# Performance work log

Hardware: AMD Instinct MI355X
Metric: run time of the kernel (lower is better)

The kernel has to match this reference:

```python
import jax, jax.numpy as jnp
import numpy as np

B, N, D = 2, 2048, 1024
H, DH = 16, 64
THETA = 10000.0


def setup_inputs() -> dict:
    key = jax.random.key(0)
    k1, k2, k3, k4 = jax.random.split(key, 4)
    hidden_states = jax.random.normal(k1, (B, N, D), dtype=jnp.float32)
    # to_qkv: Linear(D, 3*H*DH, bias=False); stored as [in, out]
    w_qkv = jax.random.normal(k2, (D, 3 * H * DH), dtype=jnp.float32) * (1.0 / np.sqrt(D))
    # to_out: Linear(H*DH, D) with bias (torch default)
    w_out = jax.random.normal(k3, (H * DH, D), dtype=jnp.float32) * (1.0 / np.sqrt(H * DH))
    b_out = jax.random.normal(k4, (D,), dtype=jnp.float32) * 0.01
    return {"hidden_states": hidden_states, "w_qkv": w_qkv, "w_out": w_out, "b_out": b_out}


def _rope_cos_sin(n, dh, dtype):
    # lucidrains RotaryEmbedding: interleaved pairs, theta=10000
    inv_freq = 1.0 / (THETA ** (jnp.arange(0, dh, 2, dtype=jnp.float32) / dh))  # [dh/2]
    t = jnp.arange(n, dtype=jnp.float32)
    freqs = t[:, None] * inv_freq[None, :]                 # [n, dh/2]
    freqs = jnp.repeat(freqs, 2, axis=-1)                  # [n, dh] interleaved
    return jnp.cos(freqs).astype(dtype), jnp.sin(freqs).astype(dtype)


def _rotate_half(x):
    # interleaved: (..., d) -> pairs (x1, x2) -> (-x2, x1)
    x = x.reshape(*x.shape[:-1], -1, 2)
    x1, x2 = x[..., 0], x[..., 1]
    return jnp.stack([-x2, x1], axis=-1).reshape(*x.shape[:-2], -1)


def reference(hidden_states, w_qkv, w_out, b_out):
    b, n, d = hidden_states.shape
    qkv = hidden_states @ w_qkv                            # [b, n, 3*H*DH]
    q, k, v = jnp.split(qkv, 3, axis=-1)
    # b n (h d) -> b h n d
    to_heads = lambda t: t.reshape(b, n, H, DH).transpose(0, 2, 1, 3)
    q, k, v = to_heads(q), to_heads(k), to_heads(v)
    cos, sin = _rope_cos_sin(n, DH, q.dtype)               # [n, DH]
    q = q * cos + _rotate_half(q) * sin
    k = k * cos + _rotate_half(k) * sin
    scale = 1.0 / np.sqrt(DH)
    scores = jnp.einsum('bhqd,bhkd->bhqk', q, k) * scale   # [b, h, n, n]
    attn = jax.nn.softmax(scores, axis=-1)
    out = jnp.einsum('bhqk,bhkd->bhqd', attn, v)           # [b, h, n, DH]
    out = out.transpose(0, 2, 1, 3).reshape(b, n, H * DH)  # b h n d -> b n (h d)
    return out @ w_out + b_out
```

## Files before the change

### kernel.cpp

```cpp
#include <hip/hip_runtime.h>
#include <hip/hip_bf16.h>

typedef __bf16 bf16;
typedef unsigned int u32;
typedef __attribute__((ext_vector_type(4))) float f32x4;
typedef __attribute__((ext_vector_type(16))) float f32x16;
typedef __attribute__((ext_vector_type(8))) bf16 bf16x8;
typedef __attribute__((ext_vector_type(4))) bf16 bf16x4;
typedef __attribute__((ext_vector_type(2))) bf16 bf16x2;
typedef __attribute__((ext_vector_type(4))) u32 u32x4;
typedef __attribute__((ext_vector_type(2))) u32 u32x2;

#define GPTR(p) ((const __attribute__((address_space(1))) u32*)(p))
#define SPTR(p) ((__attribute__((address_space(3))) u32*)(p))

#if __has_builtin(__builtin_amdgcn_permlane32_swap)
#define HAVE_PLSWAP 1
#else
#define HAVE_PLSWAP 0
#endif
#if __has_builtin(__builtin_amdgcn_fdot2_f32_bf16)
#define HAVE_DOT2 1
#else
#define HAVE_DOT2 0
#endif

constexpr int BATCH = 2, SEQ = 2048, DMODEL = 1024, NH = 16, HD = 64, QKV3 = 3072;
constexpr int MTOK = BATCH * SEQ;

constexpr size_t OXB = 0;
constexpr size_t OWQ = OXB + (size_t)MTOK * DMODEL * 2;
constexpr size_t OWO = OWQ + (size_t)QKV3 * DMODEL * 2;
constexpr size_t OCS = OWO + (size_t)DMODEL * DMODEL * 2;
constexpr size_t OCQ = OCS + (size_t)SEQ * 32 * 8;
constexpr size_t OQR = OCQ + (size_t)MTOK * QKV3 * 2;
constexpr size_t OKR = OQR + (size_t)BATCH * NH * SEQ * HD * 2;
constexpr size_t OVT = OKR + (size_t)BATCH * NH * SEQ * HD * 2;
constexpr size_t OAO = OXB;

static __device__ __forceinline__ bf16 tobf(float x) { return (bf16)x; }
static __device__ __forceinline__ float tof(bf16 x) { return (float)x; }

static __device__ __forceinline__ f32x4 mfma16(bf16x8 a, bf16x8 b, f32x4 c) {
  return __builtin_amdgcn_mfma_f32_16x16x32_bf16(a, b, c, 0, 0, 0);
}
static __device__ __forceinline__ f32x16 mfma32(bf16x8 a, bf16x8 b, f32x16 c) {
  return __builtin_amdgcn_mfma_f32_32x32x16_bf16(a, b, c, 0, 0, 0);
}

__global__ void k_prep(const float* __restrict__ hs, const float* __restrict__ wqkv,
                       float* __restrict__ cs, bf16* __restrict__ Xb,
                       bf16* __restrict__ Wqkt) {
  __shared__ float tile[32][33];
  int blk = blockIdx.x, tid = threadIdx.x;
  if (blk < 256) {
    int idx = blk * 256 + tid;
    int n = idx >> 5, i = idx & 31;
    float freq = powf(10000.0f, -(float)(2 * i) / 64.0f);
    float ang = (float)n * freq;
    float s, c;
    sincosf(ang, &s, &c);
    cs[idx * 2] = c;
    cs[idx * 2 + 1] = s;
  } else if (blk < 256 + 4096) {
    int i = (blk - 256) * 256 + tid;
    float4 v = ((const float4*)hs)[i];
    bf16x4 o = {tobf(v.x), tobf(v.y), tobf(v.z), tobf(v.w)};
    ((bf16x4*)Xb)[i] = o;
  } else {
    int t = blk - 4352;
    int n0 = (t % 96) * 32, k0 = (t / 96) * 32;
    int tx = tid & 31, ty = tid >> 5;
#pragma unroll
    for (int r = ty; r < 32; r += 8) tile[r][tx] = wqkv[(size_t)(k0 + r) * QKV3 + n0 + tx];
    __syncthreads();
#pragma unroll
    for (int r = ty; r < 32; r += 8) Wqkt[(size_t)(n0 + r) * DMODEL + k0 + tx] = tobf(tile[tx][r]);
  }
}


__global__ __launch_bounds__(256) void k_gemm2(const bf16* __restrict__ A, const bf16* __restrict__ Bt,
                                               float* __restrict__ C, const float* __restrict__ bias,
                                               int M, int Nn, int K) {
  __shared__ __attribute__((aligned(16))) char smem[36864];
  const int nTn = Nn >> 7;
  int nwg = gridDim.x;
  int bid = blockIdx.x;
  int wgs = (bid & 7) * (nwg >> 3) + (bid >> 3);
  const int m0 = (wgs / nTn) << 6;
  const int n0 = (wgs % nTn) << 7;
  const int tid = threadIdx.x;
  const int lane = tid & 63, w = tid >> 6;
  const int wr = w >> 1, wc = w & 1;
  const int l15 = lane & 15, lhi = lane >> 4;
  f32x4 acc[2][4] = {};

  const int fA = tid * 16;
  const int rA = fA >> 6;
  const int keA = (((fA & 63) >> 4) ^ ((rA >> 1) & 3)) << 3;
  const int fB0 = tid * 16, fB1 = fB0 + 4096;
  const int rB0 = fB0 >> 6, rB1 = fB1 >> 6;
  const int keB0 = (((fB0 & 63) >> 4) ^ ((rB0 >> 1) & 3)) << 3;
  const int keB1 = (((fB1 & 63) >> 4) ^ ((rB1 >> 1) & 3)) << 3;
  const int rsw = ((l15 >> 1) & 3) << 3;

#define GSTAGE(bb_, k0_)                                                                       \
  do {                                                                                         \
    __builtin_amdgcn_global_load_lds(GPTR(A + (size_t)(m0 + rA) * K + (k0_) + keA),            \
                                     SPTR(smem + (bb_)*12288 + fA), 16, 0, 0);                 \
    __builtin_amdgcn_global_load_lds(GPTR(Bt + (size_t)(n0 + rB0) * K + (k0_) + keB0),         \
                                     SPTR(smem + (bb_)*12288 + 4096 + fB0), 16, 0, 0);         \
    __builtin_amdgcn_global_load_lds(GPTR(Bt + (size_t)(n0 + rB1) * K + (k0_) + keB1),         \
                                     SPTR(smem + (bb_)*12288 + 4096 + fB1), 16, 0, 0);         \
  } while (0)

  GSTAGE(0, 0);
  GSTAGE(1, 32);
  const int nIt = K >> 5;
  int bi = 0, b2 = 2;
  for (int it = 0; it < nIt; ++it) {
    if (it < nIt - 1) {
      asm volatile("s_waitcnt vmcnt(3)" ::: "memory");
    } else {
      asm volatile("s_waitcnt vmcnt(0)" ::: "memory");
    }
    __builtin_amdgcn_s_barrier();
    if (it + 2 < nIt) GSTAGE(b2, (it + 2) << 5);
    const bf16* As = (const bf16*)(smem + bi * 12288);
    const bf16* Bs = (const bf16*)(smem + bi * 12288 + 4096);
    bf16x8 af[2], bfv[4];
#pragma unroll
    for (int i = 0; i < 2; ++i)
      af[i] = *(const bf16x8*)(As + (wr * 32 + i * 16 + l15) * 32 + ((lhi << 3) ^ rsw));
#pragma unroll
    for (int j = 0; j < 4; ++j)
      bfv[j] = *(const bf16x8*)(Bs + (wc * 64 + j * 16 + l15) * 32 + ((lhi << 3) ^ rsw));
    __builtin_amdgcn_s_setprio(1);
#pragma unroll
    for (int i = 0; i < 2; ++i)
#pragma unroll
      for (int j = 0; j < 4; ++j) acc[i][j] = mfma16(af[i], bfv[j], acc[i][j]);
    __builtin_amdgcn_s_setprio(0);
    bi = (bi == 2) ? 0 : bi + 1;
    b2 = (b2 == 2) ? 0 : b2 + 1;
  }
#undef GSTAGE

  float bj[4];
#pragma unroll
  for (int j = 0; j < 4; ++j) bj[j] = bias[n0 + wc * 64 + j * 16 + l15];
#pragma unroll
  for (int i = 0; i < 2; ++i)
#pragma unroll
    for (int j = 0; j < 4; ++j) {
      int row = m0 + wr * 32 + i * 16 + lhi * 4;
      int col = n0 + wc * 64 + j * 16 + l15;
#pragma unroll
      for (int r = 0; r < 4; ++r) C[(size_t)(row + r) * Nn + col] = acc[i][j][r] + bj[j];
    }
}


__global__ __launch_bounds__(256) void k_gemm1f(const bf16* __restrict__ A, const bf16* __restrict__ Bt,
                                                const float* __restrict__ cs,
                                                const float* __restrict__ wout, bf16* __restrict__ Woutt,
                                                bf16* __restrict__ Qr, bf16* __restrict__ Kr,
                                                bf16* __restrict__ Vt) {
  constexpr int K = DMODEL, Nn = QKV3;
  constexpr int NG = (MTOK / 128) * (QKV3 / 128);
  __shared__ __attribute__((aligned(16))) char smem[49152];
  int bid = blockIdx.x;
  const int tid = threadIdx.x;

  if (bid >= NG) {
    float* tile = (float*)smem;
    int t = bid - NG;
    int n0 = (t & 31) * 32, k0 = (t >> 5) * 32;
    int tx = tid & 31, ty = tid >> 5;
#pragma unroll
    for (int r = ty; r < 32; r += 8) tile[r * 33 + tx] = wout[(size_t)(k0 + r) * DMODEL + n0 + tx];
    __syncthreads();
#pragma unroll
    for (int r = ty; r < 32; r += 8) Woutt[(size_t)(n0 + r) * DMODEL + k0 + tx] = tobf(tile[tx * 33 + r]);
    return;
  }

  const int nTn = Nn >> 7;
  int wgs = (bid & 7) * (NG >> 3) + (bid >> 3);
  const int m0 = (wgs / nTn) << 7;
  const int n0 = (wgs % nTn) << 7;
  const int lane = tid & 63, w = tid >> 6;
  const int wr = w >> 1, wc = w & 1;
  const int l15 = lane & 15, lhi = lane >> 4;
  f32x4 acc[4][4] = {};

  const int flat0 = w * 1024 + lane * 16;
  const int flat1 = flat0 + 4096;
  const int row0 = flat0 >> 6, row1 = flat1 >> 6;
  const int ke0 = (((flat0 & 63) >> 4) ^ ((row0 >> 1) & 3)) << 3;
  const int ke1 = (((flat1 & 63) >> 4) ^ ((row1 >> 1) & 3)) << 3;
  const int rsw = ((l15 >> 1) & 3) << 3;

#define GSTAGE(bb_, k0_)                                                                       \
  do {                                                                                         \
    __builtin_amdgcn_global_load_lds(GPTR(A + (size_t)(m0 + row0) * K + (k0_) + ke0),          \
                                     SPTR(smem + (bb_)*16384 + flat0), 16, 0, 0);              \
    __builtin_amdgcn_global_load_lds(GPTR(A + (size_t)(m0 + row1) * K + (k0_) + ke1),          \
                                     SPTR(smem + (bb_)*16384 + flat1), 16, 0, 0);              \
    __builtin_amdgcn_global_load_lds(GPTR(Bt + (size_t)(n0 + row0) * K + (k0_) + ke0),         \
                                     SPTR(smem + (bb_)*16384 + 8192 + flat0), 16, 0, 0);       \
    __builtin_amdgcn_global_load_lds(GPTR(Bt + (size_t)(n0 + row1) * K + (k0_) + ke1),         \
                                     SPTR(smem + (bb_)*16384 + 8192 + flat1), 16, 0, 0);       \
  } while (0)

  GSTAGE(0, 0);
  GSTAGE(1, 32);
  const int nIt = K >> 5;
  int bi = 0, b2 = 2;
  for (int it = 0; it < nIt; ++it) {
    if (it < nIt - 1) {
      asm volatile("s_waitcnt vmcnt(4)" ::: "memory");
    } else {
      asm volatile("s_waitcnt vmcnt(0)" ::: "memory");
    }
    __builtin_amdgcn_s_barrier();
    if (it + 2 < nIt) GSTAGE(b2, (it + 2) << 5);
    const bf16* As = (const bf16*)(smem + bi * 16384);
    const bf16* Bs = (const bf16*)(smem + bi * 16384 + 8192);
    bf16x8 af[4], bfv[4];
#pragma unroll
    for (int i = 0; i < 4; ++i) {
      af[i] = *(const bf16x8*)(As + (wr * 64 + i * 16 + l15) * 32 + ((lhi << 3) ^ rsw));
      bfv[i] = *(const bf16x8*)(Bs + (wc * 64 + i * 16 + l15) * 32 + ((lhi << 3) ^ rsw));
    }
    __builtin_amdgcn_s_setprio(1);
#pragma unroll
    for (int i = 0; i < 4; ++i)
#pragma unroll
      for (int j = 0; j < 4; ++j) acc[i][j] = mfma16(af[i], bfv[j], acc[i][j]);
    __builtin_amdgcn_s_setprio(0);
    bi = (bi == 2) ? 0 : bi + 1;
    b2 = (b2 == 2) ? 0 : b2 + 1;
  }
#undef GSTAGE

  __syncthreads();
  const int part = n0 >> 10;
  const int b = m0 >> 11;

  if (part < 2) {
    bf16* Cs = (bf16*)smem;
#pragma unroll
    for (int i = 0; i < 4; ++i)
#pragma unroll
      for (int j = 0; j < 4; ++j) {
        int row = wr * 64 + i * 16 + lhi * 4;
        int col = wc * 64 + j * 16 + l15;
#pragma unroll
        for (int r = 0; r < 4; ++r) Cs[(row + r) * 128 + col] = tobf(acc[i][j][r]);
      }
    __syncthreads();
    bf16* dst = part == 0 ? Qr : Kr;
#pragma unroll
    for (int inst = 0; inst < 8; ++inst) {
      int flat = inst * 4096 + tid * 16;
      int row = flat >> 8, c0 = (flat & 255) >> 1;
      int n = (m0 + row) & 2047;
      int gc = (n0 & 1023) + c0;
      int h = gc >> 6, d0 = gc & 63;
      u32x4 v = *(const u32x4*)(smem + flat);
      const float* cp = cs + (((n << 5) + (d0 >> 1)) << 1);
      f32x4 csA = *(const f32x4*)cp;
      f32x4 csB = *(const f32x4*)(cp + 4);
      u32x4 ow;
#pragma unroll
      for (int j = 0; j < 4; ++j) {
        float cc = (j == 0) ? csA[0] : (j == 1) ? csA[2] : (j == 2) ? csB[0] : csB[2];
        float sn = (j == 0) ? csA[1] : (j == 1) ? csA[3] : (j == 2) ? csB[1] : csB[3];
        u32 pw = v[j];
        u32 tl = pw << 16, th = pw & 0xffff0000u;
        float a0, a1;
        __builtin_memcpy(&a0, &tl, 4);
        __builtin_memcpy(&a1, &th, 4);
        bf16 o0 = tobf(a0 * cc - a1 * sn);
        bf16 o1 = tobf(a1 * cc + a0 * sn);
        unsigned short u0, u1;
        __builtin_memcpy(&u0, &o0, 2);
        __builtin_memcpy(&u1, &o1, 2);
        ow[j] = (u32)u0 | ((u32)u1 << 16);
      }
      *(u32x4*)(dst + (((size_t)(b * 16 + h) * 2048 + n) << 6) + d0) = ow;
    }
  } else {
#pragma unroll
    for (int i = 0; i < 4; ++i)
#pragma unroll
      for (int j = 0; j < 4; ++j) {
        int col = wc * 64 + j * 16 + l15;
#pragma unroll
        for (int r = 0; r < 4; ++r) {
          int row = wr * 64 + i * 16 + lhi * 4 + r;
          int byte = (col << 8) + ((((row >> 3) ^ (col & 7)) << 4) | ((row & 7) << 1));
          *(bf16*)(smem + byte) = tobf(acc[i][j][r]);
        }
      }
    __syncthreads();
#pragma unroll
    for (int inst = 0; inst < 8; ++inst) {
      int flat = inst * 4096 + tid * 16;
      int c = flat >> 8;
      int rr0 = (flat & 255) >> 1;
      u32x4 vv = *(const u32x4*)(smem + (c << 8) + ((((rr0 >> 3) ^ (c & 7)) << 4)));
      int gc = (n0 & 1023) + c;
      int h = gc >> 6, dd = gc & 63;
      *(u32x4*)(Vt + (((size_t)(b * 16 + h) * 64 + dd) << 11) + (m0 & 2047) + rr0) = vv;
    }
  }
}

__global__ __launch_bounds__(512, 4) void k_attn(const bf16* __restrict__ Qr,
                                                 const bf16* __restrict__ Kr,
                                                 const bf16* __restrict__ Vt,
                                                 bf16* __restrict__ AO) {
  __shared__ __attribute__((aligned(16))) char lds[2][40960];
  int wg = blockIdx.x;
  int work = (wg & 7) * 64 + (wg >> 3);
  int qc = work & 15, h = (work >> 4) & 15, b = work >> 8;
  int tid = threadIdx.x;
  int wv = tid >> 6, lane = tid & 63;
  int pipe = wv >> 2, wsub = wv & 3;
  int l31 = lane & 31, h5 = lane >> 5;
  int q0 = qc * 128 + wsub * 32;
  int kbase = pipe << 10;
  const bf16* Qb = Qr + ((size_t)(b * NH + h)) * SEQ * 64;
  const bf16* Kb = Kr + ((size_t)(b * NH + h)) * SEQ * 64;
  const bf16* Vb = Vt + ((size_t)(b * NH + h)) * 64 * SEQ;
  char* pb = lds[pipe];

  int ptid = tid & 255;
  int sf0 = ptid * 16, sf1 = 4096 + ptid * 16;
  int sr0 = sf0 >> 7, sr1 = sf1 >> 7;
  int sc0 = (sf0 & 127) ^ ((sr0 & 7) << 4);
  int sc1 = (sf1 & 127) ^ ((sr1 & 7) << 4);
  size_t kgb0 = (size_t)sr0 * 64 + (sc0 >> 1), kgb1 = (size_t)sr1 * 64 + (sc1 >> 1);
  size_t vgb0 = (size_t)sr0 * SEQ + (sc0 >> 1), vgb1 = (size_t)sr1 * SEQ + (sc1 >> 1);

#define STAGE_K(bi_, kb_)                                                                     \
  do {                                                                                        \
    size_t ko_ = (size_t)(kbase + (kb_));                                                     \
    char* bb_ = pb + (bi_)*8192;                                                              \
    __builtin_amdgcn_global_load_lds(GPTR(Kb + ko_ * 64 + kgb0), SPTR(bb_ + sf0), 16, 0, 0);  \
    __builtin_amdgcn_global_load_lds(GPTR(Kb + ko_ * 64 + kgb1), SPTR(bb_ + sf1), 16, 0, 0);  \
  } while (0)
#define STAGE_V(bi_, kb_)                                                                     \
  do {                                                                                        \
    size_t ko_ = (size_t)(kbase + (kb_));                                                     \
    char* bb_ = pb + 24576 + (bi_)*8192;                                                      \
    __builtin_amdgcn_global_load_lds(GPTR(Vb + ko_ + vgb0), SPTR(bb_ + sf0), 16, 0, 0);       \
    __builtin_amdgcn_global_load_lds(GPTR(Vb + ko_ + vgb1), SPTR(bb_ + sf1), 16, 0, 0);       \
  } while (0)

  bf16x8 qf[4];
#pragma unroll
  for (int s = 0; s < 4; ++s) qf[s] = *(const bf16x8*)(Qb + (q0 + l31) * 64 + s * 16 + h5 * 8);

  f32x16 acc0 = {}, acc1 = {};
#if HAVE_DOT2
  float sacc0 = 0.f, sacc1 = 0.f, sacc2 = 0.f, sacc3 = 0.f;
  const bf16x2 ones2 = {(bf16)1.0f, (bf16)1.0f};
#else
  float ssum_run = 0.f;
#endif
  const float sc = 0.125f * 1.44269504f;
  const float FOFF = 8.0f;
  const int sw = (l31 & 7) << 4;
  const int cbase = h5 * 16;

  STAGE_K(0, 0);
  STAGE_V(0, 0);
  STAGE_K(1, 64);

  constexpr int NT = (SEQ / 2) / 64;
  int kc = 0, kc2 = 2;
  for (int t = 0; t < NT; ++t) {
    if (t < NT - 1) {
      asm volatile("s_waitcnt vmcnt(2)" ::: "memory");
    } else {
      asm volatile("s_waitcnt vmcnt(0)" ::: "memory");
    }
    __builtin_amdgcn_s_barrier();
    if (t + 1 < NT) STAGE_V((t + 1) & 1, (t + 1) * 64);
    if (t + 2 < NT) STAGE_K(kc2, (t + 2) * 64);
    char* cbK = pb + kc * 8192;
    char* cbV = pb + 24576 + (t & 1) * 8192;
    kc = (kc == 2) ? 0 : kc + 1;
    kc2 = (kc2 == 2) ? 0 : kc2 + 1;

    f32x16 st0 = {}, st1 = {};
    __builtin_amdgcn_s_setprio(1);
#pragma unroll
    for (int s = 0; s < 4; ++s) {
      bf16x8 kf0 = *(const bf16x8*)(cbK + l31 * 128 + ((s * 32 + cbase) ^ sw));
      bf16x8 kf1 = *(const bf16x8*)(cbK + 4096 + l31 * 128 + ((s * 32 + cbase) ^ sw));
      st0 = mfma32(kf0, qf[s], st0);
      st1 = mfma32(kf1, qf[s], st1);
    }
    __builtin_amdgcn_s_setprio(0);

    float p[32];
#pragma unroll
    for (int r = 0; r < 16; ++r) p[r] = __builtin_amdgcn_exp2f(fmaf(st0[r], sc, -FOFF));
#pragma unroll
    for (int r = 0; r < 16; ++r) p[16 + r] = __builtin_amdgcn_exp2f(fmaf(st1[r], sc, -FOFF));

    u32 P32[16];
#pragma unroll
    for (int i = 0; i < 16; ++i) {
      bf16 lo = tobf(p[2 * i]), hi = tobf(p[2 * i + 1]);
      unsigned short ul, uh;
      __builtin_memcpy(&ul, &lo, 2);
      __builtin_memcpy(&uh, &hi, 2);
      P32[i] = (u32)ul | ((u32)uh << 16);
    }

#if HAVE_DOT2
#pragma unroll
    for (int i = 0; i < 16; i += 4) {
      sacc0 = __builtin_amdgcn_fdot2_f32_bf16(__builtin_bit_cast(bf16x2, P32[i]), ones2, sacc0, false);
      sacc1 = __builtin_amdgcn_fdot2_f32_bf16(__builtin_bit_cast(bf16x2, P32[i + 1]), ones2, sacc1, false);
      sacc2 = __builtin_amdgcn_fdot2_f32_bf16(__builtin_bit_cast(bf16x2, P32[i + 2]), ones2, sacc2, false);
      sacc3 = __builtin_amdgcn_fdot2_f32_bf16(__builtin_bit_cast(bf16x2, P32[i + 3]), ones2, sacc3, false);
    }
#else
    {
      float sm[16];
#pragma unroll
      for (int i = 0; i < 16; ++i) {
        u32 ulo = P32[i] << 16, uhi = P32[i] & 0xffff0000u;
        float flo, fhi;
        __builtin_memcpy(&flo, &ulo, 4);
        __builtin_memcpy(&fhi, &uhi, 4);
        sm[i] = flo + fhi;
      }
#pragma unroll
      for (int off = 8; off > 0; off >>= 1)
#pragma unroll
        for (int r = 0; r < off; ++r) sm[r] += sm[r + off];
      ssum_run += sm[0];
    }
#endif

#if !HAVE_PLSWAP
    const int evens[8] = {0, 1, 4, 5, 8, 9, 12, 13};
    const int odds[8] = {2, 3, 6, 7, 10, 11, 14, 15};
    u32 recv[8];
#pragma unroll
    for (int j = 0; j < 8; ++j) {
      u32 sv = h5 ? P32[evens[j]] : P32[odds[j]];
      recv[j] = (u32)__shfl_xor((int)sv, 32, 64);
    }
#endif

    __builtin_amdgcn_s_setprio(1);
#pragma unroll
    for (int s2 = 0; s2 < 4; ++s2) {
      int x0 = ((s2 >> 1) << 3) + ((s2 & 1) << 2);
#if HAVE_PLSWAP
      u32x2 r02 = __builtin_amdgcn_permlane32_swap(P32[x0], P32[x0 + 2], false, false);
      u32x2 r13 = __builtin_amdgcn_permlane32_swap(P32[x0 + 1], P32[x0 + 3], false, false);
      u32x4 wv4 = {r02.x, r13.x, r02.y, r13.y};
#else
      u32 w0 = h5 ? recv[2 * s2] : P32[x0];
      u32 w1 = h5 ? recv[2 * s2 + 1] : P32[x0 + 1];
      u32 w2 = h5 ? P32[x0 + 2] : recv[2 * s2];
      u32 w3 = h5 ? P32[x0 + 3] : recv[2 * s2 + 1];
      u32x4 wv4 = {w0, w1, w2, w3};
#endif
      bf16x8 pfr = __builtin_bit_cast(bf16x8, wv4);
      bf16x8 vf0 = *(const bf16x8*)(cbV + l31 * 128 + ((s2 * 32 + cbase) ^ sw));
      bf16x8 vf1 = *(const bf16x8*)(cbV + 4096 + l31 * 128 + ((s2 * 32 + cbase) ^ sw));
      acc0 = mfma32(vf0, pfr, acc0);
      acc1 = mfma32(vf1, pfr, acc1);
    }
    __builtin_amdgcn_s_setprio(0);
  }

#if HAVE_DOT2
  float ssum = (sacc0 + sacc1) + (sacc2 + sacc3);
#else
  float ssum = ssum_run;
#endif

  __syncthreads();
  float* cacc = (float*)&lds[0][0];
  float* csum = (float*)(&lds[0][0] + 36864);
  int slot = (wsub * 64 + lane) * 36;
  if (pipe == 1) {
#pragma unroll
    for (int r = 0; r < 16; r += 4) {
      *(f32x4*)(cacc + slot + r) = f32x4{acc0[r], acc0[r + 1], acc0[r + 2], acc0[r + 3]};
      *(f32x4*)(cacc + slot + 16 + r) = f32x4{acc1[r], acc1[r + 1], acc1[r + 2], acc1[r + 3]};
    }
    csum[wsub * 64 + lane] = ssum;
  }
  __syncthreads();
  if (pipe == 0) {
#pragma unroll
    for (int r = 0; r < 16; r += 4) {
      f32x4 v0 = *(const f32x4*)(cacc + slot + r);
      f32x4 v1 = *(const f32x4*)(cacc + slot + 16 + r);
#pragma unroll
      for (int j = 0; j < 4; ++j) { acc0[r + j] += v0[j]; acc1[r + j] += v1[j]; }
    }
    ssum += csum[wsub * 64 + lane];
    ssum += __shfl_xor(ssum, 32, 64);
    float inv = 1.0f / ssum;
    size_t tok = (size_t)(b * SEQ + q0 + l31);
#pragma unroll
    for (int a = 0; a < 4; ++a) {
      bf16x4 ov0, ov1;
#pragma unroll
      for (int j = 0; j < 4; ++j) {
        ov0[j] = tobf(acc0[4 * a + j] * inv);
        ov1[j] = tobf(acc1[4 * a + j] * inv);
      }
      *(bf16x4*)(AO + tok * (NH * HD) + h * 64 + 8 * a + 4 * h5) = ov0;
      *(bf16x4*)(AO + tok * (NH * HD) + h * 64 + 32 + 8 * a + 4 * h5) = ov1;
    }
  }
#undef STAGE_K
#undef STAGE_V
}


extern "C" void kernel_launch(void* const* d_in, const int* in_sizes, int n_in,
                              void* d_out, int out_size, void* d_ws, size_t ws_size,
                              hipStream_t stream) {
  const float* hs = (const float*)d_in[0];
  const float* wqkv = (const float*)d_in[1];
  const float* wout = (const float*)d_in[2];
  const float* bout = (const float*)d_in[3];
  char* ws = (char*)d_ws;
  bf16* Xb = (bf16*)(ws + OXB);
  bf16* Wqkt = (bf16*)(ws + OWQ);
  bf16* Woutt = (bf16*)(ws + OWO);
  float* cs = (float*)(ws + OCS);
  bf16* Qr = (bf16*)(ws + OQR);
  bf16* Kr = (bf16*)(ws + OKR);
  bf16* Vt = (bf16*)(ws + OVT);
  bf16* AO = (bf16*)(ws + OAO);

  k_prep<<<7424, 256, 0, stream>>>(hs, wqkv, cs, Xb, Wqkt);
  k_gemm1f<<<(MTOK / 128) * (QKV3 / 128) + 1024, 256, 0, stream>>>(Xb, Wqkt, cs, wout, Woutt, Qr, Kr, Vt);
  k_attn<<<BATCH * NH * (SEQ / 128), 512, 0, stream>>>(Qr, Kr, Vt, AO);
  k_gemm2<<<(MTOK / 64) * (DMODEL / 128), 256, 0, stream>>>(AO, Woutt, (float*)d_out, bout, MTOK, DMODEL, DMODEL);
}
```

Before: 115.2 us.

## Drop split-KV pipes in attention; each block handles 256 queries over full sequence

Attention blocks previously split the key range into two pipes of four waves each and reduced partial accumulators through LDS. Now all eight waves cover distinct query rows (256 per block) and iterate over the full key sequence with one shared K/V staging buffer. This removes the LDS cross-pipe reduction and halves per-block LDS, and K/V tiles are now reused across twice as many queries. In exchange the grid halves to 256 blocks, and each block runs a loop twice as long.

```diff
diff --git a/kernel.cpp b/kernel.cpp
--- a/kernel.cpp
+++ b/kernel.cpp
@@ -319,46 +319,38 @@
   }
 }
 
-__global__ __launch_bounds__(512, 4) void k_attn(const bf16* __restrict__ Qr,
+__global__ __launch_bounds__(512, 8) void k_attn(const bf16* __restrict__ Qr,
                                                  const bf16* __restrict__ Kr,
                                                  const bf16* __restrict__ Vt,
                                                  bf16* __restrict__ AO) {
-  __shared__ __attribute__((aligned(16))) char lds[2][40960];
+  __shared__ __attribute__((aligned(16))) char lds[40960];
   int wg = blockIdx.x;
-  int work = (wg & 7) * 64 + (wg >> 3);
-  int qc = work & 15, h = (work >> 4) & 15, b = work >> 8;
+  int work = (wg & 7) * 32 + (wg >> 3);
+  int qc = work & 7, h = (work >> 3) & 15, b = work >> 7;
   int tid = threadIdx.x;
   int wv = tid >> 6, lane = tid & 63;
-  int pipe = wv >> 2, wsub = wv & 3;
   int l31 = lane & 31, h5 = lane >> 5;
-  int q0 = qc * 128 + wsub * 32;
-  int kbase = pipe << 10;
+  int q0 = qc * 256 + wv * 32;
   const bf16* Qb = Qr + ((size_t)(b * NH + h)) * SEQ * 64;
   const bf16* Kb = Kr + ((size_t)(b * NH + h)) * SEQ * 64;
   const bf16* Vb = Vt + ((size_t)(b * NH + h)) * 64 * SEQ;
-  char* pb = lds[pipe];
-
-  int ptid = tid & 255;
-  int sf0 = ptid * 16, sf1 = 4096 + ptid * 16;
-  int sr0 = sf0 >> 7, sr1 = sf1 >> 7;
+  char* pb = lds;
+
+  int sf0 = tid * 16;
+  int sr0 = sf0 >> 7;
   int sc0 = (sf0 & 127) ^ ((sr0 & 7) << 4);
-  int sc1 = (sf1 & 127) ^ ((sr1 & 7) << 4);
-  size_t kgb0 = (size_t)sr0 * 64 + (sc0 >> 1), kgb1 = (size_t)sr1 * 64 + (sc1 >> 1);
-  size_t vgb0 = (size_t)sr0 * SEQ + (sc0 >> 1), vgb1 = (size_t)sr1 * SEQ + (sc1 >> 1);
+  size_t kgb0 = (size_t)sr0 * 64 + (sc0 >> 1);
+  size_t vgb0 = (size_t)sr0 * SEQ + (sc0 >> 1);
 
 #define STAGE_K(bi_, kb_)                                                                     \
   do {                                                                                        \
-    size_t ko_ = (size_t)(kbase + (kb_));                                                     \
     char* bb_ = pb + (bi_)*8192;                                                              \
-    __builtin_amdgcn_global_load_lds(GPTR(Kb + ko_ * 64 + kgb0), SPTR(bb_ + sf0), 16, 0, 0);  \
-    __builtin_amdgcn_global_load_lds(GPTR(Kb + ko_ * 64 + kgb1), SPTR(bb_ + sf1), 16, 0, 0);  \
+    __builtin_amdgcn_global_load_lds(GPTR(Kb + (size_t)(kb_)*64 + kgb0), SPTR(bb_ + sf0), 16, 0, 0); \
   } while (0)
 #define STAGE_V(bi_, kb_)                                                                     \
   do {                                                                                        \
-    size_t ko_ = (size_t)(kbase + (kb_));                                                     \
     char* bb_ = pb + 24576 + (bi_)*8192;                                                      \
-    __builtin_amdgcn_global_load_lds(GPTR(Vb + ko_ + vgb0), SPTR(bb_ + sf0), 16, 0, 0);       \
-    __builtin_amdgcn_global_load_lds(GPTR(Vb + ko_ + vgb1), SPTR(bb_ + sf1), 16, 0, 0);       \
+    __builtin_amdgcn_global_load_lds(GPTR(Vb + (size_t)(kb_) + vgb0), SPTR(bb_ + sf0), 16, 0, 0); \
   } while (0)
 
   bf16x8 qf[4];
@@ -381,11 +373,11 @@
   STAGE_V(0, 0);
   STAGE_K(1, 64);
 
-  constexpr int NT = (SEQ / 2) / 64;
+  constexpr int NT = SEQ / 64;
   int kc = 0, kc2 = 2;
   for (int t = 0; t < NT; ++t) {
     if (t < NT - 1) {
-      asm volatile("s_waitcnt vmcnt(2)" ::: "memory");
+      asm volatile("s_waitcnt vmcnt(1)" ::: "memory");
     } else {
       asm volatile("s_waitcnt vmcnt(0)" ::: "memory");
     }
@@ -492,42 +484,19 @@
   float ssum = ssum_run;
 #endif
 
-  __syncthreads();
-  float* cacc = (float*)&lds[0][0];
-  float* csum = (float*)(&lds[0][0] + 36864);
-  int slot = (wsub * 64 + lane) * 36;
-  if (pipe == 1) {
-#pragma unroll
-    for (int r = 0; r < 16; r += 4) {
-      *(f32x4*)(cacc + slot + r) = f32x4{acc0[r], acc0[r + 1], acc0[r + 2], acc0[r + 3]};
-      *(f32x4*)(cacc + slot + 16 + r) = f32x4{acc1[r], acc1[r + 1], acc1[r + 2], acc1[r + 3]};
-    }
-    csum[wsub * 64 + lane] = ssum;
-  }
-  __syncthreads();
-  if (pipe == 0) {
-#pragma unroll
-    for (int r = 0; r < 16; r += 4) {
-      f32x4 v0 = *(const f32x4*)(cacc + slot + r);
-      f32x4 v1 = *(const f32x4*)(cacc + slot + 16 + r);
-#pragma unroll
-      for (int j = 0; j < 4; ++j) { acc0[r + j] += v0[j]; acc1[r + j] += v1[j]; }
-    }
-    ssum += csum[wsub * 64 + lane];
-    ssum += __shfl_xor(ssum, 32, 64);
-    float inv = 1.0f / ssum;
-    size_t tok = (size_t)(b * SEQ + q0 + l31);
-#pragma unroll
-    for (int a = 0; a < 4; ++a) {
-      bf16x4 ov0, ov1;
-#pragma unroll
-      for (int j = 0; j < 4; ++j) {
-        ov0[j] = tobf(acc0[4 * a + j] * inv);
-        ov1[j] = tobf(acc1[4 * a + j] * inv);
-      }
-      *(bf16x4*)(AO + tok * (NH * HD) + h * 64 + 8 * a + 4 * h5) = ov0;
-      *(bf16x4*)(AO + tok * (NH * HD) + h * 64 + 32 + 8 * a + 4 * h5) = ov1;
-    }
+  ssum += __shfl_xor(ssum, 32, 64);
+  float inv = 1.0f / ssum;
+  size_t tok = (size_t)(b * SEQ + q0 + l31);
+#pragma unroll
+  for (int a = 0; a < 4; ++a) {
+    bf16x4 ov0, ov1;
+#pragma unroll
+    for (int j = 0; j < 4; ++j) {
+      ov0[j] = tobf(acc0[4 * a + j] * inv);
+      ov1[j] = tobf(acc1[4 * a + j] * inv);
+    }
+    *(bf16x4*)(AO + tok * (NH * HD) + h * 64 + 8 * a + 4 * h5) = ov0;
+    *(bf16x4*)(AO + tok * (NH * HD) + h * 64 + 32 + 8 * a + 4 * h5) = ov1;
   }
 #undef STAGE_K
 #undef STAGE_V
@@ -553,6 +522,6 @@
 
   k_prep<<<7424, 256, 0, stream>>>(hs, wqkv, cs, Xb, Wqkt);
   k_gemm1f<<<(MTOK / 128) * (QKV3 / 128) + 1024, 256, 0, stream>>>(Xb, Wqkt, cs, wout, Woutt, Qr, Kr, Vt);
-  k_attn<<<BATCH * NH * (SEQ / 128), 512, 0, stream>>>(Qr, Kr, Vt, AO);
+  k_attn<<<BATCH * NH * (SEQ / 256), 512, 0, stream>>>(Qr, Kr, Vt, AO);
   k_gemm2<<<(MTOK / 64) * (DMODEL / 128), 256, 0, stream>>>(AO, Woutt, (float*)d_out, bout, MTOK, DMODEL, DMODEL);
 }
```

Measured after the change: 277.0 us. 140% more time.

## Split attention key range across four wave pipes with 1024-thread blocks

Applied to the files above, without the earlier changes.

Doubles the attention workgroup to 1024 threads so four pipes of four waves each process a quarter of the key sequence, using 32-key tiles per step instead of 64. Each pipe streams less K/V through smaller LDS buffers, and a two-level LDS tree reduction merges the partial accumulators and row sums. The aim is more concurrent waves per query block, hiding memory and exp latency better. The cost is extra reduction barriers, half-size MFMA work per iteration, and a possible occupancy or register limit from the 1024-thread launch bound.

```diff
diff --git a/kernel.cpp b/kernel.cpp
--- a/kernel.cpp
+++ b/kernel.cpp
@@ -319,11 +319,11 @@
   }
 }
 
-__global__ __launch_bounds__(512, 4) void k_attn(const bf16* __restrict__ Qr,
-                                                 const bf16* __restrict__ Kr,
-                                                 const bf16* __restrict__ Vt,
-                                                 bf16* __restrict__ AO) {
-  __shared__ __attribute__((aligned(16))) char lds[2][40960];
+__global__ __launch_bounds__(1024, 4) void k_attn(const bf16* __restrict__ Qr,
+                                                  const bf16* __restrict__ Kr,
+                                                  const bf16* __restrict__ Vt,
+                                                  bf16* __restrict__ AO) {
+  __shared__ __attribute__((aligned(16))) char lds[4][20480];
   int wg = blockIdx.x;
   int work = (wg & 7) * 64 + (wg >> 3);
   int qc = work & 15, h = (work >> 4) & 15, b = work >> 8;
@@ -332,33 +332,30 @@
   int pipe = wv >> 2, wsub = wv & 3;
   int l31 = lane & 31, h5 = lane >> 5;
   int q0 = qc * 128 + wsub * 32;
-  int kbase = pipe << 10;
+  int kbase = pipe << 9;
   const bf16* Qb = Qr + ((size_t)(b * NH + h)) * SEQ * 64;
   const bf16* Kb = Kr + ((size_t)(b * NH + h)) * SEQ * 64;
   const bf16* Vb = Vt + ((size_t)(b * NH + h)) * 64 * SEQ;
   char* pb = lds[pipe];
 
   int ptid = tid & 255;
-  int sf0 = ptid * 16, sf1 = 4096 + ptid * 16;
-  int sr0 = sf0 >> 7, sr1 = sf1 >> 7;
-  int sc0 = (sf0 & 127) ^ ((sr0 & 7) << 4);
-  int sc1 = (sf1 & 127) ^ ((sr1 & 7) << 4);
-  size_t kgb0 = (size_t)sr0 * 64 + (sc0 >> 1), kgb1 = (size_t)sr1 * 64 + (sc1 >> 1);
-  size_t vgb0 = (size_t)sr0 * SEQ + (sc0 >> 1), vgb1 = (size_t)sr1 * SEQ + (sc1 >> 1);
+  int sf0 = ptid * 16;
+  int srk = sf0 >> 7;
+  int sck = (sf0 & 127) ^ ((srk & 7) << 4);
+  size_t kgb0 = (size_t)srk * 64 + (sck >> 1);
+  size_t vgb0 = (size_t)(sf0 >> 6) * SEQ + ((sf0 & 63) >> 1);
 
 #define STAGE_K(bi_, kb_)                                                                     \
   do {                                                                                        \
-    size_t ko_ = (size_t)(kbase + (kb_));                                                     \
-    char* bb_ = pb + (bi_)*8192;                                                              \
-    __builtin_amdgcn_global_load_lds(GPTR(Kb + ko_ * 64 + kgb0), SPTR(bb_ + sf0), 16, 0, 0);  \
-    __builtin_amdgcn_global_load_lds(GPTR(Kb + ko_ * 64 + kgb1), SPTR(bb_ + sf1), 16, 0, 0);  \
+    char* bb_ = pb + (bi_)*4096;                                                              \
+    __builtin_amdgcn_global_load_lds(GPTR(Kb + (size_t)(kbase + (kb_)) * 64 + kgb0),          \
+                                     SPTR(bb_ + sf0), 16, 0, 0);                              \
   } while (0)
 #define STAGE_V(bi_, kb_)                                                                     \
   do {                                                                                        \
-    size_t ko_ = (size_t)(kbase + (kb_));                                                     \
-    char* bb_ = pb + 24576 + (bi_)*8192;                                                      \
-    __builtin_amdgcn_global_load_lds(GPTR(Vb + ko_ + vgb0), SPTR(bb_ + sf0), 16, 0, 0);       \
-    __builtin_amdgcn_global_load_lds(GPTR(Vb + ko_ + vgb1), SPTR(bb_ + sf1), 16, 0, 0);       \
+    char* bb_ = pb + 12288 + (bi_)*4096;                                                      \
+    __builtin_amdgcn_global_load_lds(GPTR(Vb + (size_t)(kbase + (kb_)) + vgb0),               \
+                                     SPTR(bb_ + sf0), 16, 0, 0);                              \
   } while (0)
 
   bf16x8 qf[4];
@@ -379,45 +376,38 @@
 
   STAGE_K(0, 0);
   STAGE_V(0, 0);
-  STAGE_K(1, 64);
-
-  constexpr int NT = (SEQ / 2) / 64;
+  STAGE_K(1, 32);
+
+  constexpr int NT = (SEQ / 4) / 32;
   int kc = 0, kc2 = 2;
   for (int t = 0; t < NT; ++t) {
     if (t < NT - 1) {
-      asm volatile("s_waitcnt vmcnt(2)" ::: "memory");
+      asm volatile("s_waitcnt vmcnt(1)" ::: "memory");
     } else {
       asm volatile("s_waitcnt vmcnt(0)" ::: "memory");
     }
     __builtin_amdgcn_s_barrier();
-    if (t + 1 < NT) STAGE_V((t + 1) & 1, (t + 1) * 64);
-    if (t + 2 < NT) STAGE_K(kc2, (t + 2) * 64);
-    char* cbK = pb + kc * 8192;
-    char* cbV = pb + 24576 + (t & 1) * 8192;
+    if (t + 1 < NT) STAGE_V((t + 1) & 1, (t + 1) * 32);
+    if (t + 2 < NT) STAGE_K(kc2, (t + 2) * 32);
+    char* cbK = pb + kc * 4096;
+    char* cbV = pb + 12288 + (t & 1) * 4096;
     kc = (kc == 2) ? 0 : kc + 1;
     kc2 = (kc2 == 2) ? 0 : kc2 + 1;
 
-    f32x16 st0 = {}, st1 = {};
+    f32x16 st = {};
     __builtin_amdgcn_s_setprio(1);
 #pragma unroll
     for (int s = 0; s < 4; ++s) {
-      bf16x8 kf0 = *(const bf16x8*)(cbK + l31 * 128 + ((s * 32 + cbase) ^ sw));
-      bf16x8 kf1 = *(const bf16x8*)(cbK + 4096 + l31 * 128 + ((s * 32 + cbase) ^ sw));
-      st0 = mfma32(kf0, qf[s], st0);
-      st1 = mfma32(kf1, qf[s], st1);
+      bf16x8 kf = *(const bf16x8*)(cbK + l31 * 128 + ((s * 32 + cbase) ^ sw));
+      st = mfma32(kf, qf[s], st);
     }
     __builtin_amdgcn_s_setprio(0);
 
-    float p[32];
-#pragma unroll
-    for (int r = 0; r < 16; ++r) p[r] = __builtin_amdgcn_exp2f(fmaf(st0[r], sc, -FOFF));
-#pragma unroll
-    for (int r = 0; r < 16; ++r) p[16 + r] = __builtin_amdgcn_exp2f(fmaf(st1[r], sc, -FOFF));
-
-    u32 P32[16];
-#pragma unroll
-    for (int i = 0; i < 16; ++i) {
-      bf16 lo = tobf(p[2 * i]), hi = tobf(p[2 * i + 1]);
+    u32 P32[8];
+#pragma unroll
+    for (int i = 0; i < 8; ++i) {
+      bf16 lo = tobf(__builtin_amdgcn_exp2f(fmaf(st[2 * i], sc, -FOFF)));
+      bf16 hi = tobf(__builtin_amdgcn_exp2f(fmaf(st[2 * i + 1], sc, -FOFF)));
       unsigned short ul, uh;
       __builtin_memcpy(&ul, &lo, 2);
       __builtin_memcpy(&uh, &hi, 2);
@@ -426,7 +416,7 @@
 
 #if HAVE_DOT2
 #pragma unroll
-    for (int i = 0; i < 16; i += 4) {
+    for (int i = 0; i < 8; i += 4) {
       sacc0 = __builtin_amdgcn_fdot2_f32_bf16(__builtin_bit_cast(bf16x2, P32[i]), ones2, sacc0, false);
       sacc1 = __builtin_amdgcn_fdot2_f32_bf16(__builtin_bit_cast(bf16x2, P32[i + 1]), ones2, sacc1, false);
       sacc2 = __builtin_amdgcn_fdot2_f32_bf16(__builtin_bit_cast(bf16x2, P32[i + 2]), ones2, sacc2, false);
@@ -434,9 +424,9 @@
     }
 #else
     {
-      float sm[16];
-#pragma unroll
-      for (int i = 0; i < 16; ++i) {
+      float sm[8];
+#pragma unroll
+      for (int i = 0; i < 8; ++i) {
         u32 ulo = P32[i] << 16, uhi = P32[i] & 0xffff0000u;
         float flo, fhi;
         __builtin_memcpy(&flo, &ulo, 4);
@@ -444,7 +434,7 @@
         sm[i] = flo + fhi;
       }
 #pragma unroll
-      for (int off = 8; off > 0; off >>= 1)
+      for (int off = 4; off > 0; off >>= 1)
 #pragma unroll
         for (int r = 0; r < off; ++r) sm[r] += sm[r + off];
       ssum_run += sm[0];
@@ -452,20 +442,20 @@
 #endif
 
 #if !HAVE_PLSWAP
-    const int evens[8] = {0, 1, 4, 5, 8, 9, 12, 13};
-    const int odds[8] = {2, 3, 6, 7, 10, 11, 14, 15};
-    u32 recv[8];
-#pragma unroll
-    for (int j = 0; j < 8; ++j) {
-      u32 sv = h5 ? P32[evens[j]] : P32[odds[j]];
+    const int sndA[4] = {2, 3, 6, 7};
+    const int sndB[4] = {0, 1, 4, 5};
+    u32 recv[4];
+#pragma unroll
+    for (int j = 0; j < 4; ++j) {
+      u32 sv = h5 ? P32[sndB[j]] : P32[sndA[j]];
       recv[j] = (u32)__shfl_xor((int)sv, 32, 64);
     }
 #endif
 
     __builtin_amdgcn_s_setprio(1);
 #pragma unroll
-    for (int s2 = 0; s2 < 4; ++s2) {
-      int x0 = ((s2 >> 1) << 3) + ((s2 & 1) << 2);
+    for (int s2 = 0; s2 < 2; ++s2) {
+      int x0 = s2 * 4;
 #if HAVE_PLSWAP
       u32x2 r02 = __builtin_amdgcn_permlane32_swap(P32[x0], P32[x0 + 2], false, false);
       u32x2 r13 = __builtin_amdgcn_permlane32_swap(P32[x0 + 1], P32[x0 + 3], false, false);
@@ -478,8 +468,8 @@
       u32x4 wv4 = {w0, w1, w2, w3};
 #endif
       bf16x8 pfr = __builtin_bit_cast(bf16x8, wv4);
-      bf16x8 vf0 = *(const bf16x8*)(cbV + l31 * 128 + ((s2 * 32 + cbase) ^ sw));
-      bf16x8 vf1 = *(const bf16x8*)(cbV + 4096 + l31 * 128 + ((s2 * 32 + cbase) ^ sw));
+      bf16x8 vf0 = *(const bf16x8*)(cbV + l31 * 64 + s2 * 32 + cbase);
+      bf16x8 vf1 = *(const bf16x8*)(cbV + 2048 + l31 * 64 + s2 * 32 + cbase);
       acc0 = mfma32(vf0, pfr, acc0);
       acc1 = mfma32(vf1, pfr, acc1);
     }
@@ -493,27 +483,49 @@
 #endif
 
   __syncthreads();
-  float* cacc = (float*)&lds[0][0];
-  float* csum = (float*)(&lds[0][0] + 36864);
+  float* R0 = (float*)&lds[0][0];
+  float* R1 = R0 + 9216;
   int slot = (wsub * 64 + lane) * 36;
-  if (pipe == 1) {
+  if (pipe == 1 || pipe == 3) {
+    float* R = (pipe == 1) ? R0 : R1;
 #pragma unroll
     for (int r = 0; r < 16; r += 4) {
-      *(f32x4*)(cacc + slot + r) = f32x4{acc0[r], acc0[r + 1], acc0[r + 2], acc0[r + 3]};
-      *(f32x4*)(cacc + slot + 16 + r) = f32x4{acc1[r], acc1[r + 1], acc1[r + 2], acc1[r + 3]};
-    }
-    csum[wsub * 64 + lane] = ssum;
+      *(f32x4*)(R + slot + r) = f32x4{acc0[r], acc0[r + 1], acc0[r + 2], acc0[r + 3]};
+      *(f32x4*)(R + slot + 16 + r) = f32x4{acc1[r], acc1[r + 1], acc1[r + 2], acc1[r + 3]};
+    }
+    R[slot + 32] = ssum;
+  }
+  __syncthreads();
+  if (pipe == 0 || pipe == 2) {
+    float* R = (pipe == 0) ? R0 : R1;
+#pragma unroll
+    for (int r = 0; r < 16; r += 4) {
+      f32x4 v0 = *(const f32x4*)(R + slot + r);
+      f32x4 v1 = *(const f32x4*)(R + slot + 16 + r);
+#pragma unroll
+      for (int j = 0; j < 4; ++j) { acc0[r + j] += v0[j]; acc1[r + j] += v1[j]; }
+    }
+    ssum += R[slot + 32];
+  }
+  __syncthreads();
+  if (pipe == 2) {
+#pragma unroll
+    for (int r = 0; r < 16; r += 4) {
+      *(f32x4*)(R0 + slot + r) = f32x4{acc0[r], acc0[r + 1], acc0[r + 2], acc0[r + 3]};
+      *(f32x4*)(R0 + slot + 16 + r) = f32x4{acc1[r], acc1[r + 1], acc1[r + 2], acc1[r + 3]};
+    }
+    R0[slot + 32] = ssum;
   }
   __syncthreads();
   if (pipe == 0) {
 #pragma unroll
     for (int r = 0; r < 16; r += 4) {
-      f32x4 v0 = *(const f32x4*)(cacc + slot + r);
-      f32x4 v1 = *(const f32x4*)(cacc + slot + 16 + r);
+      f32x4 v0 = *(const f32x4*)(R0 + slot + r);
+      f32x4 v1 = *(const f32x4*)(R0 + slot + 16 + r);
 #pragma unroll
       for (int j = 0; j < 4; ++j) { acc0[r + j] += v0[j]; acc1[r + j] += v1[j]; }
     }
-    ssum += csum[wsub * 64 + lane];
+    ssum += R0[slot + 32];
     ssum += __shfl_xor(ssum, 32, 64);
     float inv = 1.0f / ssum;
     size_t tok = (size_t)(b * SEQ + q0 + l31);
@@ -553,6 +565,6 @@
 
   k_prep<<<7424, 256, 0, stream>>>(hs, wqkv, cs, Xb, Wqkt);
   k_gemm1f<<<(MTOK / 128) * (QKV3 / 128) + 1024, 256, 0, stream>>>(Xb, Wqkt, cs, wout, Woutt, Qr, Kr, Vt);
-  k_attn<<<BATCH * NH * (SEQ / 128), 512, 0, stream>>>(Qr, Kr, Vt, AO);
+  k_attn<<<BATCH * NH * (SEQ / 128), 1024, 0, stream>>>(Qr, Kr, Vt, AO);
   k_gemm2<<<(MTOK / 64) * (DMODEL / 128), 256, 0, stream>>>(AO, Woutt, (float*)d_out, bout, MTOK, DMODEL, DMODEL);
 }
```

Result: slower. 120.8 us (+4.8%).
